# Optimization experiments

Measured on AMD Instinct MI355X. Metric: run time of the kernel, lower is better.

Reference implementation:

```python
import jax, jax.numpy as jnp
import numpy as np

# Collage decoder constants (from init_kwargs)
RES = 256          # config.data_res
C = 3              # collage_width
RH = RW = 8        # range patch size
DH = DW = 64       # domain patch size
N_DH = RES // DH   # 4 domain patches per side
N_D = N_DH * N_DH  # 16 domain patches
N_RH = RES // RH   # 32 range patches per side
N_R = N_RH * N_RH  # 1024 range patches
HF = DH // RH      # 8: pooling factor domain->range size
STEPS = 10


def setup_inputs() -> dict:
    key = jax.random.key(0)
    k1, k2, k3 = jax.random.split(key, 3)
    patch_emb = jax.random.normal(k1, (8, RH, RW, 256), dtype=jnp.float32)
    # get_1x1(theta_width): 1x1 conv == channel matmul, weight (256, 147456)
    w_theta = jax.random.normal(k2, (256, N_R * 3 * N_D * C), dtype=jnp.float32) * 0.01
    b_theta = jax.random.normal(k3, (N_R * 3 * N_D * C,), dtype=jnp.float32) * 0.01
    return {"patch_emb": patch_emb, "w_theta": w_theta, "b_theta": b_theta}


def reference(patch_emb, w_theta, b_theta):
    bs = patch_emb.shape[0]
    # patch_to_theta (1x1 conv) then avg_pool over full spatial extent -> (bs, theta_width)
    theta = jnp.einsum('bhwk,kt->bhwt', patch_emb, w_theta) + b_theta
    theta = theta.mean(axis=(1, 2))
    theta = theta.reshape(bs, 3 * N_R, N_D, C)
    mul, add, mix = jnp.split(theta, 3, axis=1)       # each (bs, N_R, N_D, C)
    mix = jax.nn.softmax(mix, axis=1)                 # softmax over range-patch axis (axis=1)
    mul = jnp.tanh(mul) * mix
    add = jnp.tanh(add) * mix
    add_sum = add.sum(axis=2)                         # (bs, N_R, C)

    iterate = jnp.zeros((bs, RES, RES, C), dtype=patch_emb.dtype)
    for _ in range(STEPS):
        # partition_img: gather domain patches -> (bs, N_D, DH, DW, C)
        d = iterate.reshape(bs, N_DH, DH, N_DH, DW, C)
        d = d.transpose(0, 1, 3, 2, 4, 5).reshape(bs, N_D, DH, DW, C)
        # reduce: mean-pool each domain patch down to range size (bs, N_D, RH, RW, C)
        d = d.reshape(bs, N_D, RH, HF, RW, HF, C).mean(axis=(3, 5))
        # affine combine: soft collage links every range to every domain
        out = jnp.einsum('brdc,bdhwc->brhwc', mul, d) + add_sum[:, :, None, None, :]
        iterate = out.reshape(bs, N_RH, N_RH, RH, RW, C)
        iterate = iterate.transpose(0, 1, 3, 2, 4, 5).reshape(bs, RES, RES, C)
    return iterate
```

## Files before the change

### kernel.cpp

```cpp
#include <hip/hip_runtime.h>
#include <math.h>

#define T_COLS 147456
#define BS 8
#define NU 49152

#define OFF_ME      0
#define OFF_THETA   2048
#define OFF_MULP    (OFF_THETA + BS*T_COLS)
#define OFF_ADDSUM  (OFF_MULP + 8*3*1024*16)
#define OFF_Q       (OFF_ADDSUM + 8*3*1024)

__device__ __forceinline__ float tanh_fast(float x) {
    float e = __expf(2.f * x);
    return 1.f - 2.f * __builtin_amdgcn_rcpf(e + 1.f);
}

__global__ __launch_bounds__(1024) void k1_mean(const float* __restrict__ pe,
                                                float* __restrict__ me) {
    int b = blockIdx.x;
    int k = threadIdx.x & 255, qd = threadIdx.x >> 8;
    const float* p = pe + (size_t)b * 16384 + qd * 4096 + k;
    float s = 0.f;
#pragma unroll
    for (int i = 0; i < 16; i++) s += p[i * 256];
    __shared__ float part[4][256];
    part[qd][k] = s;
    __syncthreads();
    if (threadIdx.x < 256) {
        float v = part[0][k] + part[1][k] + part[2][k] + part[3][k];
        me[k * 8 + b] = v * (1.f / 64.f);
    }
}

__global__ __launch_bounds__(192) void k2_gemm(const float* __restrict__ w,
                                               const float* __restrict__ bt,
                                               const float* __restrict__ me,
                                               float* __restrict__ tt) {
    __shared__ __align__(16) float lme[2048];
    __shared__ float lt[8][192];
    int tid = threadIdx.x;
    for (int i = tid; i < 2048; i += 192) lme[i] = me[i];
    __syncthreads();

    int t = blockIdx.x * 192 + tid;
    const float* wp = w + t;
    float acc[8];
#pragma unroll
    for (int b = 0; b < 8; b++) acc[b] = 0.f;

#pragma unroll 16
    for (int k = 0; k < 256; k++) {
        float wv = wp[(size_t)k * T_COLS];
        const float4* m4 = reinterpret_cast<const float4*>(&lme[k * 8]);
        float4 m0 = m4[0], m1 = m4[1];
        acc[0] += m0.x * wv;
        acc[1] += m0.y * wv;
        acc[2] += m0.z * wv;
        acc[3] += m0.w * wv;
        acc[4] += m1.x * wv;
        acc[5] += m1.y * wv;
        acc[6] += m1.z * wv;
        acc[7] += m1.w * wv;
    }
    float bv = bt[t];
#pragma unroll
    for (int b = 0; b < 8; b++) lt[b][tid] = acc[b] + bv;
    __syncthreads();

    int u0 = blockIdx.x * 64;
    int j = tid & 63;
    int c = tid >> 6;
#pragma unroll
    for (int b = 0; b < 8; b++) {
        float v = lt[b][j * 3 + c];
        tt[(size_t)(b * 3 + c) * NU + u0 + j] = v;
    }
}

#define MVL_STRIDE 1028
__global__ __launch_bounds__(1024) void kC(const float* __restrict__ tt,
                                           float* __restrict__ mulp,
                                           float* __restrict__ addsum,
                                           float* __restrict__ q) {
    int bc = blockIdx.x;
    int r = threadIdx.x;
    int lane = r & 63, wv = r >> 6;
    const float4* base = reinterpret_cast<const float4*>(tt + (size_t)bc * NU);

    __shared__ float redm[16 * 16];
    __shared__ float gm[16], ginv[16];
    __shared__ float mvl[16 * MVL_STRIDE];
    __shared__ float sred[1024];
    __shared__ float Ash[256];
    __shared__ float svl[16], pl[16];

    float mx[16];
    {
        float4 x0 = base[8192 + r * 4 + 0];
        float4 x1 = base[8192 + r * 4 + 1];
        float4 x2 = base[8192 + r * 4 + 2];
        float4 x3 = base[8192 + r * 4 + 3];
        mx[0] = x0.x; mx[1] = x0.y; mx[2] = x0.z; mx[3] = x0.w;
        mx[4] = x1.x; mx[5] = x1.y; mx[6] = x1.z; mx[7] = x1.w;
        mx[8] = x2.x; mx[9] = x2.y; mx[10] = x2.z; mx[11] = x2.w;
        mx[12] = x3.x; mx[13] = x3.y; mx[14] = x3.z; mx[15] = x3.w;
    }
    {
        float wred[16];
#pragma unroll
        for (int d = 0; d < 16; d++) wred[d] = mx[d];
#pragma unroll
        for (int m = 32; m > 0; m >>= 1)
#pragma unroll
            for (int d = 0; d < 16; d++)
                wred[d] = fmaxf(wred[d], __shfl_xor(wred[d], m));
        if (lane == 0) {
#pragma unroll
            for (int d = 0; d < 16; d++) redm[wv * 16 + d] = wred[d];
        }
    }
    __syncthreads();
    if (r < 16) {
        float m = -1e30f;
#pragma unroll
        for (int w = 0; w < 16; w++) m = fmaxf(m, redm[w * 16 + r]);
        gm[r] = m;
    }
    __syncthreads();

    {
        float wred[16];
#pragma unroll
        for (int d = 0; d < 16; d++) {
            mx[d] = __expf(mx[d] - gm[d]);
            wred[d] = mx[d];
        }
#pragma unroll
        for (int m = 32; m > 0; m >>= 1)
#pragma unroll
            for (int d = 0; d < 16; d++)
                wred[d] += __shfl_xor(wred[d], m);
        if (lane == 0) {
#pragma unroll
            for (int d = 0; d < 16; d++) redm[wv * 16 + d] = wred[d];
        }
    }
    __syncthreads();
    if (r < 16) {
        float s = 0.f;
#pragma unroll
        for (int w = 0; w < 16; w++) s += redm[w * 16 + r];
        ginv[r] = 1.f / s;
    }
    __syncthreads();
#pragma unroll
    for (int d = 0; d < 16; d++) mx[d] *= ginv[d];

    float asum = 0.f;
    {
        float4 a0 = base[4096 + r * 4 + 0];
        float4 a1 = base[4096 + r * 4 + 1];
        float4 a2 = base[4096 + r * 4 + 2];
        float4 a3 = base[4096 + r * 4 + 3];
        float av[16];
        av[0] = a0.x; av[1] = a0.y; av[2] = a0.z; av[3] = a0.w;
        av[4] = a1.x; av[5] = a1.y; av[6] = a1.z; av[7] = a1.w;
        av[8] = a2.x; av[9] = a2.y; av[10] = a2.z; av[11] = a2.w;
        av[12] = a3.x; av[13] = a3.y; av[14] = a3.z; av[15] = a3.w;
#pragma unroll
        for (int d = 0; d < 16; d++) asum += tanh_fast(av[d]) * mx[d];
    }
    addsum[(size_t)bc * 1024 + r] = asum;
    sred[r] = asum;

    float mv[16];
    {
        float4 m0 = base[r * 4 + 0];
        float4 m1 = base[r * 4 + 1];
        float4 m2 = base[r * 4 + 2];
        float4 m3 = base[r * 4 + 3];
        mv[0] = m0.x; mv[1] = m0.y; mv[2] = m0.z; mv[3] = m0.w;
        mv[4] = m1.x; mv[5] = m1.y; mv[6] = m1.z; mv[7] = m1.w;
        mv[8] = m2.x; mv[9] = m2.y; mv[10] = m2.z; mv[11] = m2.w;
        mv[12] = m3.x; mv[13] = m3.y; mv[14] = m3.z; mv[15] = m3.w;
#pragma unroll
        for (int d = 0; d < 16; d++) mv[d] = tanh_fast(mv[d]) * mx[d];
    }
    {
        float4* mp = reinterpret_cast<float4*>(&mulp[((size_t)bc * 1024 + r) * 16]);
        mp[0] = make_float4(mv[0], mv[1], mv[2], mv[3]);
        mp[1] = make_float4(mv[4], mv[5], mv[6], mv[7]);
        mp[2] = make_float4(mv[8], mv[9], mv[10], mv[11]);
        mp[3] = make_float4(mv[12], mv[13], mv[14], mv[15]);
    }
#pragma unroll
    for (int d = 0; d < 16; d++) mvl[d * MVL_STRIDE + r] = mv[d];
    __syncthreads();

    if (r < 256) {
        int dd = r >> 4, d = r & 15;
        int di = dd >> 2, dj = dd & 3;
        const float* bse = &mvl[d * MVL_STRIDE + di * 256 + dj * 8];
        float s = 0.f;
        for (int a = 0; a < 8; a++) {
#pragma unroll
            for (int e = 0; e < 8; e++) s += bse[a * 32 + e];
        }
        Ash[r] = s * (1.f / 64.f);
    }
    if (r < 16) {
        int di = r >> 2, dj = r & 3;
        float s = 0.f;
        for (int a = 0; a < 8; a++)
#pragma unroll
            for (int e = 0; e < 8; e++) s += sred[di * 256 + a * 32 + dj * 8 + e];
        svl[r] = s * (1.f / 64.f);
    }
    __syncthreads();

    if (r < 64) {
        int d2 = r & 15;
        float arow[16];
#pragma unroll
        for (int d = 0; d < 16; d++) arow[d] = Ash[d2 * 16 + d];
        float sv = svl[d2];
        float pd = 0.f;
        for (int it = 0; it < 8; it++) {
            float x = sv;
#pragma unroll
            for (int d = 0; d < 16; d++) x += arow[d] * __shfl(pd, d, 16);
            pd = x;
        }
        if (r < 16) pl[r] = pd;
    }
    __syncthreads();

    {
        float x = asum;
#pragma unroll
        for (int d = 0; d < 16; d++) x += mv[d] * pl[d];
        q[(size_t)bc * 1024 + r] = x;
    }
}

__global__ __launch_bounds__(512) void k5_final(const float* __restrict__ mulp,
                                                const float* __restrict__ addsum,
                                                const float* __restrict__ q,
                                                float* __restrict__ out) {
    int blk = blockIdx.x;
    int b = blk >> 5, ri = blk & 31;
    int tid = threadIdx.x;
    __shared__ float ql[3072];
    for (int i = tid; i < 3072; i += 512) ql[i] = q[(size_t)b * 3072 + i];
    __syncthreads();

    int h = tid >> 6;
    int rj = (tid >> 1) & 31;
    int wh = tid & 1;
    int r = ri * 32 + rj;

    float mr[3][16];
    float as[3];
#pragma unroll
    for (int c = 0; c < 3; c++) {
        const float4* mp4 = reinterpret_cast<const float4*>(
            &mulp[((size_t)(b * 3 + c) * 1024 + r) * 16]);
        float4 v0 = mp4[0], v1 = mp4[1], v2 = mp4[2], v3 = mp4[3];
        mr[c][0] = v0.x; mr[c][1] = v0.y; mr[c][2] = v0.z; mr[c][3] = v0.w;
        mr[c][4] = v1.x; mr[c][5] = v1.y; mr[c][6] = v1.z; mr[c][7] = v1.w;
        mr[c][8] = v2.x; mr[c][9] = v2.y; mr[c][10] = v2.z; mr[c][11] = v2.w;
        mr[c][12] = v3.x; mr[c][13] = v3.y; mr[c][14] = v3.z; mr[c][15] = v3.w;
        as[c] = addsum[(size_t)(b * 3 + c) * 1024 + r];
    }

    float acc[3][4];
#pragma unroll
    for (int c = 0; c < 3; c++)
#pragma unroll
        for (int w = 0; w < 4; w++) acc[c][w] = as[c];

#pragma unroll
    for (int di = 0; di < 4; di++) {
        int qrow = (di * 8 + h) * 32;
#pragma unroll
        for (int dj = 0; dj < 4; dj++) {
#pragma unroll
            for (int c = 0; c < 3; c++) {
                float m = mr[c][di * 4 + dj];
                const float* qb = &ql[c * 1024 + qrow + dj * 8 + wh * 4];
                acc[c][0] += m * qb[0];
                acc[c][1] += m * qb[1];
                acc[c][2] += m * qb[2];
                acc[c][3] += m * qb[3];
            }
        }
    }

    int i = ri * 8 + h;
    int j0 = rj * 8 + wh * 4;
    float4* ob = reinterpret_cast<float4*>(
        &out[((size_t)(b * 256 + i) * 256 + j0) * 3]);
    ob[0] = make_float4(acc[0][0], acc[1][0], acc[2][0], acc[0][1]);
    ob[1] = make_float4(acc[1][1], acc[2][1], acc[0][2], acc[1][2]);
    ob[2] = make_float4(acc[2][2], acc[0][3], acc[1][3], acc[2][3]);
}

extern "C" void kernel_launch(void* const* d_in, const int* in_sizes, int n_in,
                              void* d_out, int out_size, void* d_ws, size_t ws_size,
                              hipStream_t stream) {
    const float* pe = (const float*)d_in[0];
    const float* w  = (const float*)d_in[1];
    const float* bt = (const float*)d_in[2];
    float* ws = (float*)d_ws;

    float* me     = ws + OFF_ME;
    float* tt     = ws + OFF_THETA;
    float* mulp   = ws + OFF_MULP;
    float* addsum = ws + OFF_ADDSUM;
    float* q      = ws + OFF_Q;
    float* out = (float*)d_out;

    k1_mean<<<8, 1024, 0, stream>>>(pe, me);
    k2_gemm<<<T_COLS / 192, 192, 0, stream>>>(w, bt, me, tt);
    kC<<<24, 1024, 0, stream>>>(tt, mulp, addsum, q);
    k5_final<<<256, 512, 0, stream>>>(mulp, addsum, q, out);
}
```

Before: 61.10 us.

## Split-K the theta GEMM with float4 weight loads and a separate reduce kernel

The weight GEMM (256 x 147456 by 8 batch means) is split into four K-chunks. Each 64-thread block computes four adjacent columns with float4 loads and writes its partial sums to a workspace buffer. A new reduce kernel adds the partials and the bias and performs the transpose that used to sit in the GEMM. This raises parallelism and load width on the memory-bound 150 MB weight read, at the cost of writing and re-reading 4x8x147456 floats of partials and one extra launch.

```diff
diff --git a/kernel.cpp b/kernel.cpp
--- a/kernel.cpp
+++ b/kernel.cpp
@@ -4,12 +4,14 @@
 #define T_COLS 147456
 #define BS 8
 #define NU 49152
+#define KSPLIT 4
 
 #define OFF_ME      0
 #define OFF_THETA   2048
 #define OFF_MULP    (OFF_THETA + BS*T_COLS)
 #define OFF_ADDSUM  (OFF_MULP + 8*3*1024*16)
 #define OFF_Q       (OFF_ADDSUM + 8*3*1024)
+#define OFF_PART    (OFF_Q + 8*3*1024)
 
 __device__ __forceinline__ float tanh_fast(float x) {
     float e = __expf(2.f * x);
@@ -33,39 +35,65 @@
     }
 }
 
-__global__ __launch_bounds__(192) void k2_gemm(const float* __restrict__ w,
-                                               const float* __restrict__ bt,
-                                               const float* __restrict__ me,
-                                               float* __restrict__ tt) {
+__global__ __launch_bounds__(64) void k2_gemm(const float* __restrict__ w,
+                                              const float* __restrict__ me,
+                                              float* __restrict__ part) {
     __shared__ __align__(16) float lme[2048];
+    int lane = threadIdx.x;
+    for (int i = lane; i < 2048; i += 64) lme[i] = me[i];
+    __syncthreads();
+
+    int bid = blockIdx.x;
+    int s = bid & 3, cw = bid >> 2;
+    size_t col = ((size_t)cw * 64 + lane) * 4;
+    const float4* wp = reinterpret_cast<const float4*>(w + col);
+    const int k0 = s * 64;
+
+    float4 acc[8];
+#pragma unroll
+    for (int b = 0; b < 8; b++) acc[b] = make_float4(0.f, 0.f, 0.f, 0.f);
+
+#pragma unroll 16
+    for (int kk = 0; kk < 64; kk++) {
+        int k = k0 + kk;
+        float4 wv = wp[(size_t)k * (T_COLS / 4)];
+        const float4* m4 = reinterpret_cast<const float4*>(&lme[k * 8]);
+        float4 m0 = m4[0], m1 = m4[1];
+        acc[0].x += m0.x * wv.x; acc[0].y += m0.x * wv.y; acc[0].z += m0.x * wv.z; acc[0].w += m0.x * wv.w;
+        acc[1].x += m0.y * wv.x; acc[1].y += m0.y * wv.y; acc[1].z += m0.y * wv.z; acc[1].w += m0.y * wv.w;
+        acc[2].x += m0.z * wv.x; acc[2].y += m0.z * wv.y; acc[2].z += m0.z * wv.z; acc[2].w += m0.z * wv.w;
+        acc[3].x += m0.w * wv.x; acc[3].y += m0.w * wv.y; acc[3].z += m0.w * wv.z; acc[3].w += m0.w * wv.w;
+        acc[4].x += m1.x * wv.x; acc[4].y += m1.x * wv.y; acc[4].z += m1.x * wv.z; acc[4].w += m1.x * wv.w;
+        acc[5].x += m1.y * wv.x; acc[5].y += m1.y * wv.y; acc[5].z += m1.y * wv.z; acc[5].w += m1.y * wv.w;
+        acc[6].x += m1.z * wv.x; acc[6].y += m1.z * wv.y; acc[6].z += m1.z * wv.z; acc[6].w += m1.z * wv.w;
+        acc[7].x += m1.w * wv.x; acc[7].y += m1.w * wv.y; acc[7].z += m1.w * wv.z; acc[7].w += m1.w * wv.w;
+    }
+
+#pragma unroll
+    for (int b = 0; b < 8; b++) {
+        *reinterpret_cast<float4*>(&part[(size_t)(s * 8 + b) * T_COLS + col]) = acc[b];
+    }
+}
+
+__global__ __launch_bounds__(192) void kR(const float* __restrict__ part,
+                                          const float* __restrict__ bt,
+                                          float* __restrict__ tt) {
     __shared__ float lt[8][192];
     int tid = threadIdx.x;
-    for (int i = tid; i < 2048; i += 192) lme[i] = me[i];
-    __syncthreads();
-
     int t = blockIdx.x * 192 + tid;
-    const float* wp = w + t;
+    float bv = bt[t];
+
     float acc[8];
 #pragma unroll
-    for (int b = 0; b < 8; b++) acc[b] = 0.f;
-
-#pragma unroll 16
-    for (int k = 0; k < 256; k++) {
-        float wv = wp[(size_t)k * T_COLS];
-        const float4* m4 = reinterpret_cast<const float4*>(&lme[k * 8]);
-        float4 m0 = m4[0], m1 = m4[1];
-        acc[0] += m0.x * wv;
-        acc[1] += m0.y * wv;
-        acc[2] += m0.z * wv;
-        acc[3] += m0.w * wv;
-        acc[4] += m1.x * wv;
-        acc[5] += m1.y * wv;
-        acc[6] += m1.z * wv;
-        acc[7] += m1.w * wv;
-    }
-    float bv = bt[t];
-#pragma unroll
-    for (int b = 0; b < 8; b++) lt[b][tid] = acc[b] + bv;
+    for (int b = 0; b < 8; b++) acc[b] = bv;
+#pragma unroll
+    for (int s = 0; s < KSPLIT; s++) {
+#pragma unroll
+        for (int b = 0; b < 8; b++)
+            acc[b] += part[(size_t)(s * 8 + b) * T_COLS + t];
+    }
+#pragma unroll
+    for (int b = 0; b < 8; b++) lt[b][tid] = acc[b];
     __syncthreads();
 
     int u0 = blockIdx.x * 64;
@@ -319,10 +347,12 @@
     float* mulp   = ws + OFF_MULP;
     float* addsum = ws + OFF_ADDSUM;
     float* q      = ws + OFF_Q;
+    float* part   = ws + OFF_PART;
     float* out = (float*)d_out;
 
     k1_mean<<<8, 1024, 0, stream>>>(pe, me);
-    k2_gemm<<<T_COLS / 192, 192, 0, stream>>>(w, bt, me, tt);
+    k2_gemm<<<576 * KSPLIT, 64, 0, stream>>>(w, me, part);
+    kR<<<T_COLS / 192, 192, 0, stream>>>(part, bt, tt);
     kC<<<24, 1024, 0, stream>>>(tt, mulp, addsum, q);
     k5_final<<<256, 512, 0, stream>>>(mulp, addsum, q, out);
 }
```

Result: slower. 63.78 us (+4.4%).
